# Kernel tuning notes

Hardware: AMD Instinct MI355X
Metric: run time of the kernel (lower is better)

Reference implementation:

```python
import jax, jax.numpy as jnp
import numpy as np

N, F, H, E = 10000, 256, 256, 320000
TEMPERATURE = 1.0


def setup_inputs() -> dict:
    key = jax.random.key(0)
    k_x, k_ei, k_w1, k_b1, k_w2, k_b2 = jax.random.split(key, 6)
    x = jax.random.normal(k_x, (N, F), dtype=jnp.float32)
    edge_index = jax.random.randint(k_ei, (2, E), 0, N, dtype=jnp.int64)
    # PyTorch nn.Linear default init: U(-1/sqrt(fan_in), 1/sqrt(fan_in)), weight shape (out, in)
    lim1 = 1.0 / np.sqrt(2 * F)
    W1 = jax.random.uniform(k_w1, (H, 2 * F), dtype=jnp.float32, minval=-lim1, maxval=lim1)
    b1 = jax.random.uniform(k_b1, (H,), dtype=jnp.float32, minval=-lim1, maxval=lim1)
    lim2 = 1.0 / np.sqrt(H)
    W2 = jax.random.uniform(k_w2, (1, H), dtype=jnp.float32, minval=-lim2, maxval=lim2)
    b2 = jax.random.uniform(k_b2, (1,), dtype=jnp.float32, minval=-lim2, maxval=lim2)
    return {"x": x, "edge_index": edge_index, "W1": W1, "b1": b1, "W2": W2, "b2": b2}


def reference(x, edge_index, W1, b1, W2, b2):
    row, col = edge_index[0], edge_index[1]
    edge_feat = jnp.concatenate([x[row], x[col]], axis=-1)  # (E, 2F)
    h = jax.nn.relu(edge_feat @ W1.T + b1)                  # (E, H)
    logits = (h @ W2.T + b2).squeeze(-1)                    # (E,)
    m = jax.nn.sigmoid(logits / max(TEMPERATURE, 1e-6))
    return m
```

## Files before the change

kernel.cpp:

```cpp
#include <hip/hip_runtime.h>
#include <hip/hip_bf16.h>


typedef __attribute__((ext_vector_type(8))) short bf16x8;
typedef __attribute__((ext_vector_type(4))) float f32x4;
typedef __attribute__((ext_vector_type(2))) float f32x2;

__device__ __forceinline__ unsigned short f2bf(float f) {
    __hip_bfloat16 h = __float2bfloat16(f);
    return *reinterpret_cast<unsigned short*>(&h);
}

__global__ __launch_bounds__(256) void convert_w(const float* __restrict__ w1,
                                                 unsigned short* __restrict__ wb,
                                                 int nw4) {
    int i = blockIdx.x * 256 + threadIdx.x;
    if (i < nw4) {
        float4 v = ((const float4*)w1)[i];
        ushort4 o = {f2bf(v.x), f2bf(v.y), f2bf(v.z), f2bf(v.w)};
        ((ushort4*)wb)[i] = o;
    }
}

__global__ __launch_bounds__(512) void gemm_mfma(const float* __restrict__ x,
                                                 const unsigned short* __restrict__ wb,
                                                 const float* __restrict__ b1,
                                                 unsigned char* __restrict__ uv,
                                                 int M) {
    __shared__ __align__(16) unsigned short As[16][264];

    const int t    = threadIdx.x;
    const int wave = t >> 6;
    const int lane = t & 63;
    const int lm   = lane & 15;
    const int lq   = lane >> 4;
    const int lk   = lq * 8;
    const int m0   = blockIdx.x * 16;

    {
        const int srow = t >> 5;
        const int scol = (t & 31) * 4;
        const int gr   = m0 + srow;
        const float* xr = x + (size_t)(gr < M ? gr : (M - 1)) * 256;
#pragma unroll
        for (int i = 0; i < 2; ++i) {
            float4 v = *(const float4*)(xr + scol + i * 128);
            ushort4 o = {f2bf(v.x), f2bf(v.y), f2bf(v.z), f2bf(v.w)};
            *(ushort4*)&As[srow][scol + i * 128] = o;
        }
    }
    __syncthreads();

    const int hh = wave >> 2;
    const int r0 = (wave & 3) * 64;
    const unsigned short* bpre =
        wb + (size_t)(r0 + lm) * 512 + hh * 256 + lk;

    f32x4 acc[4];
#pragma unroll
    for (int j = 0; j < 4; ++j) acc[j] = f32x4{0.f, 0.f, 0.f, 0.f};

#pragma unroll 4
    for (int kt = 0; kt < 256; kt += 32) {
        bf16x8 xf = *(const bf16x8*)&As[lm][kt + lk];
#pragma unroll
        for (int j = 0; j < 4; ++j) {
            bf16x8 w = *(const bf16x8*)(bpre + (size_t)j * 16 * 512 + kt);
            acc[j] = __builtin_amdgcn_mfma_f32_16x16x32_bf16(w, xf, acc[j], 0, 0, 0);
        }
    }

    const int node = m0 + lm;
    if (node < M) {
        unsigned char* up = uv + (size_t)node * 512 + wave * 64 + lq * 4;
#pragma unroll
        for (int j = 0; j < 4; ++j) {
            float4 bb = (wave < 4)
                          ? *(const float4*)(b1 + wave * 64 + j * 16 + lq * 4)
                          : float4{0.f, 0.f, 0.f, 0.f};
            unsigned int d = __builtin_amdgcn_cvt_pk_fp8_f32(
                acc[j][0] + bb.x, acc[j][1] + bb.y, 0, false);
            d = __builtin_amdgcn_cvt_pk_fp8_f32(
                acc[j][2] + bb.z, acc[j][3] + bb.w, d, true);
            *(unsigned int*)(up + j * 16) = d;
        }
    }
}

__global__ __launch_bounds__(256) void edge_kernel(const unsigned char* __restrict__ uv,
                                                   const int* __restrict__ ei,
                                                   const float* __restrict__ w2,
                                                   const float* __restrict__ b2p,
                                                   float* __restrict__ out, int E) {
    const int lane = threadIdx.x & 63;
    const int g = lane >> 4;
    const int c = lane & 15;
    const int wid  = (blockIdx.x * blockDim.x + threadIdx.x) >> 6;
    const int nwav = (gridDim.x * blockDim.x) >> 6;
    const int nb   = E >> 2;

    float w2r[16];
#pragma unroll
    for (int i = 0; i < 4; ++i)
        *(float4*)&w2r[i * 4] = *(const float4*)(w2 + c * 16 + i * 4);
    const float b2 = b2p[0];

    for (int b = wid; b < nb; b += 2 * nwav) {
        const int bB = b + nwav;
        const bool has2 = bB < nb;

        const int e0 = b * 4 + g;
        const int r0 = ei[e0];
        const int c0 = ei[E + e0];
        const int e1 = has2 ? bB * 4 + g : e0;
        const int r1 = ei[e1];
        const int c1 = ei[E + e1];

        uint4 ua = *(const uint4*)(uv + (size_t)r0 * 512 + c * 16);
        uint4 va = *(const uint4*)(uv + (size_t)c0 * 512 + 256 + c * 16);
        uint4 ub = *(const uint4*)(uv + (size_t)r1 * 512 + c * 16);
        uint4 vb = *(const uint4*)(uv + (size_t)c1 * 512 + 256 + c * 16);

        unsigned int uw[4], vw[4];
        float p;

        *(uint4*)&uw[0] = ua; *(uint4*)&vw[0] = va;
        {
            float2 p2 = {0.f, 0.f};
#pragma unroll
            for (int w = 0; w < 4; ++w) {
                f32x2 u01 = __builtin_amdgcn_cvt_pk_f32_fp8(uw[w], false);
                f32x2 u23 = __builtin_amdgcn_cvt_pk_f32_fp8(uw[w], true);
                f32x2 v01 = __builtin_amdgcn_cvt_pk_f32_fp8(vw[w], false);
                f32x2 v23 = __builtin_amdgcn_cvt_pk_f32_fp8(vw[w], true);
                float s0 = fmaxf(u01.x + v01.x, 0.f);
                float s1 = fmaxf(u01.y + v01.y, 0.f);
                float s2 = fmaxf(u23.x + v23.x, 0.f);
                float s3 = fmaxf(u23.y + v23.y, 0.f);
                p2.x = fmaf(s0, w2r[4 * w + 0], p2.x);
                p2.y = fmaf(s1, w2r[4 * w + 1], p2.y);
                p2.x = fmaf(s2, w2r[4 * w + 2], p2.x);
                p2.y = fmaf(s3, w2r[4 * w + 3], p2.y);
            }
            p = p2.x + p2.y;
        }
#pragma unroll
        for (int off = 1; off < 16; off <<= 1)
            p += __shfl_xor(p, off, 64);
        if (c == 0) out[e0] = 1.f / (1.f + __expf(-(p + b2)));

        if (has2) {
            *(uint4*)&uw[0] = ub; *(uint4*)&vw[0] = vb;
            float2 p2 = {0.f, 0.f};
#pragma unroll
            for (int w = 0; w < 4; ++w) {
                f32x2 u01 = __builtin_amdgcn_cvt_pk_f32_fp8(uw[w], false);
                f32x2 u23 = __builtin_amdgcn_cvt_pk_f32_fp8(uw[w], true);
                f32x2 v01 = __builtin_amdgcn_cvt_pk_f32_fp8(vw[w], false);
                f32x2 v23 = __builtin_amdgcn_cvt_pk_f32_fp8(vw[w], true);
                float s0 = fmaxf(u01.x + v01.x, 0.f);
                float s1 = fmaxf(u01.y + v01.y, 0.f);
                float s2 = fmaxf(u23.x + v23.x, 0.f);
                float s3 = fmaxf(u23.y + v23.y, 0.f);
                p2.x = fmaf(s0, w2r[4 * w + 0], p2.x);
                p2.y = fmaf(s1, w2r[4 * w + 1], p2.y);
                p2.x = fmaf(s2, w2r[4 * w + 2], p2.x);
                p2.y = fmaf(s3, w2r[4 * w + 3], p2.y);
            }
            p = p2.x + p2.y;
#pragma unroll
            for (int off = 1; off < 16; off <<= 1)
                p += __shfl_xor(p, off, 64);
            if (c == 0) out[e1] = 1.f / (1.f + __expf(-(p + b2)));
        }
    }
}

extern "C" void kernel_launch(void* const* d_in, const int* in_sizes, int n_in,
                              void* d_out, int out_size, void* d_ws, size_t ws_size,
                              hipStream_t stream) {
    const float* x  = (const float*)d_in[0];
    const int*   ei = (const int*)d_in[1];
    const float* W1 = (const float*)d_in[2];
    const float* b1 = (const float*)d_in[3];
    const float* W2 = (const float*)d_in[4];
    const float* b2 = (const float*)d_in[5];
    float* out = (float*)d_out;

    const int N = in_sizes[0] / 256;
    const int E = in_sizes[1] / 2;

    unsigned char*  uv = (unsigned char*)d_ws;
    unsigned short* wb = (unsigned short*)(uv + (size_t)N * 512);

    const int nw4 = (256 * 512) / 4;
    convert_w<<<(nw4 + 255) / 256, 256, 0, stream>>>(W1, wb, nw4);

    dim3 g((N + 15) / 16, 1);
    gemm_mfma<<<g, 512, 0, stream>>>(x, wb, b1, uv, N);

    edge_kernel<<<2048, 256, 0, stream>>>(uv, ei, W2, b2, out, E);
}
```

Measured before the change: 114.9 us.

## Fuse weight conversion into GEMM and stage W1 half in LDS per block

Removes the separate bf16 conversion kernel for W1. The node GEMM is restructured so each 1024-thread block converts one 256x256 half of W1 into LDS and reuses it across 80 node rows, reading x directly from global and converting it in registers. This cuts one launch and the repeated global weight reads, but each block now pays for a full weight-half conversion and uses a large LDS footprint. Only 20 work items exist for 16 waves, so some waves run twice while others idle.

```diff
diff --git a/kernel.cpp b/kernel.cpp
--- a/kernel.cpp
+++ b/kernel.cpp
@@ -3,6 +3,7 @@
 
 
 typedef __attribute__((ext_vector_type(8))) short bf16x8;
+typedef __attribute__((ext_vector_type(8))) unsigned short u16x8;
 typedef __attribute__((ext_vector_type(4))) float f32x4;
 typedef __attribute__((ext_vector_type(2))) float f32x2;
 
@@ -11,78 +12,79 @@
     return *reinterpret_cast<unsigned short*>(&h);
 }
 
-__global__ __launch_bounds__(256) void convert_w(const float* __restrict__ w1,
-                                                 unsigned short* __restrict__ wb,
-                                                 int nw4) {
-    int i = blockIdx.x * 256 + threadIdx.x;
-    if (i < nw4) {
-        float4 v = ((const float4*)w1)[i];
-        ushort4 o = {f2bf(v.x), f2bf(v.y), f2bf(v.z), f2bf(v.w)};
-        ((ushort4*)wb)[i] = o;
-    }
-}
-
-__global__ __launch_bounds__(512) void gemm_mfma(const float* __restrict__ x,
-                                                 const unsigned short* __restrict__ wb,
+__global__ __launch_bounds__(1024) void gemm_lds(const float* __restrict__ x,
+                                                 const float* __restrict__ w1,
                                                  const float* __restrict__ b1,
                                                  unsigned char* __restrict__ uv,
                                                  int M) {
-    __shared__ __align__(16) unsigned short As[16][264];
+    __shared__ __align__(16) unsigned short Ws[256][264];
 
     const int t    = threadIdx.x;
     const int wave = t >> 6;
     const int lane = t & 63;
     const int lm   = lane & 15;
     const int lq   = lane >> 4;
-    const int lk   = lq * 8;
-    const int m0   = blockIdx.x * 16;
+    const int h    = blockIdx.x & 1;
+    const int c    = blockIdx.x >> 1;
 
     {
-        const int srow = t >> 5;
-        const int scol = (t & 31) * 4;
-        const int gr   = m0 + srow;
-        const float* xr = x + (size_t)(gr < M ? gr : (M - 1)) * 256;
-#pragma unroll
-        for (int i = 0; i < 2; ++i) {
-            float4 v = *(const float4*)(xr + scol + i * 128);
-            ushort4 o = {f2bf(v.x), f2bf(v.y), f2bf(v.z), f2bf(v.w)};
-            *(ushort4*)&As[srow][scol + i * 128] = o;
+        const int row = t >> 2;
+        const int col = (t & 3) * 64;
+        const float* wr = w1 + (size_t)row * 512 + h * 256 + col;
+#pragma unroll
+        for (int i = 0; i < 8; ++i) {
+            float4 a = *(const float4*)(wr + i * 8);
+            float4 b = *(const float4*)(wr + i * 8 + 4);
+            u16x8 o = {f2bf(a.x), f2bf(a.y), f2bf(a.z), f2bf(a.w),
+                       f2bf(b.x), f2bf(b.y), f2bf(b.z), f2bf(b.w)};
+            *(u16x8*)&Ws[row][col + i * 8] = o;
         }
     }
     __syncthreads();
 
-    const int hh = wave >> 2;
-    const int r0 = (wave & 3) * 64;
-    const unsigned short* bpre =
-        wb + (size_t)(r0 + lm) * 512 + hh * 256 + lk;
-
-    f32x4 acc[4];
-#pragma unroll
-    for (int j = 0; j < 4; ++j) acc[j] = f32x4{0.f, 0.f, 0.f, 0.f};
-
-#pragma unroll 4
-    for (int kt = 0; kt < 256; kt += 32) {
-        bf16x8 xf = *(const bf16x8*)&As[lm][kt + lk];
-#pragma unroll
-        for (int j = 0; j < 4; ++j) {
-            bf16x8 w = *(const bf16x8*)(bpre + (size_t)j * 16 * 512 + kt);
-            acc[j] = __builtin_amdgcn_mfma_f32_16x16x32_bf16(w, xf, acc[j], 0, 0, 0);
-        }
-    }
-
-    const int node = m0 + lm;
-    if (node < M) {
-        unsigned char* up = uv + (size_t)node * 512 + wave * 64 + lq * 4;
-#pragma unroll
-        for (int j = 0; j < 4; ++j) {
-            float4 bb = (wave < 4)
-                          ? *(const float4*)(b1 + wave * 64 + j * 16 + lq * 4)
-                          : float4{0.f, 0.f, 0.f, 0.f};
-            unsigned int d = __builtin_amdgcn_cvt_pk_fp8_f32(
-                acc[j][0] + bb.x, acc[j][1] + bb.y, 0, false);
-            d = __builtin_amdgcn_cvt_pk_fp8_f32(
-                acc[j][2] + bb.z, acc[j][3] + bb.w, d, true);
-            *(unsigned int*)(up + j * 16) = d;
+    for (int id = wave; id < 20; id += 16) {
+        const int ti = id >> 2;
+        const int q  = id & 3;
+        const int m0 = (c * 5 + ti) * 16;
+        const int r0 = q * 64;
+
+        const int gr = m0 + lm;
+        const float* xr = x + (size_t)(gr < M ? gr : (M - 1)) * 256 + lq * 8;
+
+        f32x4 acc[4];
+#pragma unroll
+        for (int j = 0; j < 4; ++j) acc[j] = f32x4{0.f, 0.f, 0.f, 0.f};
+
+#pragma unroll
+        for (int kt = 0; kt < 8; ++kt) {
+            float4 a = *(const float4*)(xr + kt * 32);
+            float4 b = *(const float4*)(xr + kt * 32 + 4);
+            bf16x8 xf;
+            xf[0] = (short)f2bf(a.x); xf[1] = (short)f2bf(a.y);
+            xf[2] = (short)f2bf(a.z); xf[3] = (short)f2bf(a.w);
+            xf[4] = (short)f2bf(b.x); xf[5] = (short)f2bf(b.y);
+            xf[6] = (short)f2bf(b.z); xf[7] = (short)f2bf(b.w);
+#pragma unroll
+            for (int j = 0; j < 4; ++j) {
+                bf16x8 wf = *(const bf16x8*)&Ws[r0 + j * 16 + lm][kt * 32 + lq * 8];
+                acc[j] = __builtin_amdgcn_mfma_f32_16x16x32_bf16(wf, xf, acc[j], 0, 0, 0);
+            }
+        }
+
+        const int node = m0 + lm;
+        if (node < M) {
+            unsigned char* up = uv + (size_t)node * 512 + h * 256 + r0 + lq * 4;
+#pragma unroll
+            for (int j = 0; j < 4; ++j) {
+                float4 bb = (h == 0)
+                              ? *(const float4*)(b1 + r0 + j * 16 + lq * 4)
+                              : float4{0.f, 0.f, 0.f, 0.f};
+                unsigned int d = __builtin_amdgcn_cvt_pk_fp8_f32(
+                    acc[j][0] + bb.x, acc[j][1] + bb.y, 0, false);
+                d = __builtin_amdgcn_cvt_pk_fp8_f32(
+                    acc[j][2] + bb.z, acc[j][3] + bb.w, d, true);
+                *(unsigned int*)(up + j * 16) = d;
+            }
         }
     }
 }
@@ -190,14 +192,10 @@
     const int N = in_sizes[0] / 256;
     const int E = in_sizes[1] / 2;
 
-    unsigned char*  uv = (unsigned char*)d_ws;
-    unsigned short* wb = (unsigned short*)(uv + (size_t)N * 512);
-
-    const int nw4 = (256 * 512) / 4;
-    convert_w<<<(nw4 + 255) / 256, 256, 0, stream>>>(W1, wb, nw4);
-
-    dim3 g((N + 15) / 16, 1);
-    gemm_mfma<<<g, 512, 0, stream>>>(x, wb, b1, uv, N);
+    unsigned char* uv = (unsigned char*)d_ws;
+
+    const int ngrp = (N + 79) / 80;
+    gemm_lds<<<ngrp * 2, 1024, 0, stream>>>(x, W1, b1, uv, N);
 
     edge_kernel<<<2048, 256, 0, stream>>>(uv, ei, W2, b2, out, E);
 }
```

After: 106.2 us (median of 2 runs). 7.6% less time.
